# Kernel tuning notes

Hardware: AMD Instinct MI355X
Metric: run time of the kernel (lower is better)

The kernel has to match this reference:

```python
import jax, jax.numpy as jnp
import numpy as np

N_NODES = 100000
N_EDGES = 625000
HIDDEN = 128
N_LAYERS = 4
NUM_GRAPHS = 512
INPUT_DIM = 28
EDGE_DIM = 4
OUT_DIM = 1


def setup_inputs() -> dict:
    key = jax.random.key(0)
    ks = jax.random.split(key, 16)
    x = jax.random.randint(ks[0], (N_NODES, 1), 0, INPUT_DIM)
    edge_index = jax.random.randint(ks[1], (2, N_EDGES), 0, N_NODES)
    edge_attr = jax.random.randint(ks[2], (N_EDGES,), 0, EDGE_DIM)
    batch = jnp.sort(jax.random.randint(ks[3], (N_NODES,), 0, NUM_GRAPHS))
    s = 1.0 / np.sqrt(HIDDEN)
    node_emb = jax.random.normal(ks[4], (INPUT_DIM, HIDDEN), jnp.float32)
    edge_emb = jax.random.normal(ks[5], (EDGE_DIM, HIDDEN), jnp.float32)
    conv_W1 = jax.random.normal(ks[6], (N_LAYERS, HIDDEN, HIDDEN), jnp.float32) * s
    conv_b1 = jnp.zeros((N_LAYERS, HIDDEN), jnp.float32)
    conv_W2 = jax.random.normal(ks[7], (N_LAYERS, HIDDEN, HIDDEN), jnp.float32) * s
    conv_b2 = jnp.zeros((N_LAYERS, HIDDEN), jnp.float32)
    mlp_W1 = jax.random.normal(ks[8], (HIDDEN, HIDDEN // 2), jnp.float32) * s
    mlp_b1 = jnp.zeros((HIDDEN // 2,), jnp.float32)
    mlp_W2 = jax.random.normal(ks[9], (HIDDEN // 2, HIDDEN // 4), jnp.float32) * (1.0 / np.sqrt(HIDDEN // 2))
    mlp_b2 = jnp.zeros((HIDDEN // 4,), jnp.float32)
    mlp_W3 = jax.random.normal(ks[10], (HIDDEN // 4, OUT_DIM), jnp.float32) * (1.0 / np.sqrt(HIDDEN // 4))
    mlp_b3 = jnp.zeros((OUT_DIM,), jnp.float32)
    return dict(x=x, edge_index=edge_index, edge_attr=edge_attr, batch=batch,
                node_emb=node_emb, edge_emb=edge_emb,
                conv_W1=conv_W1, conv_b1=conv_b1, conv_W2=conv_W2, conv_b2=conv_b2,
                mlp_W1=mlp_W1, mlp_b1=mlp_b1, mlp_W2=mlp_W2, mlp_b2=mlp_b2,
                mlp_W3=mlp_W3, mlp_b3=mlp_b3)


def reference(x, edge_index, edge_attr, batch, node_emb, edge_emb,
              conv_W1, conv_b1, conv_W2, conv_b2,
              mlp_W1, mlp_b1, mlp_W2, mlp_b2, mlp_W3, mlp_b3):
    h = node_emb[x[:, 0]]                    # [N, H] embedding lookup (x.squeeze(-1))
    _attr = edge_emb[edge_attr]              # computed in original forward but unused by GINConv
    src, dst = edge_index[0], edge_index[1]
    for l in range(N_LAYERS):
        # GINConv (eps=0): mlp((1+eps)*x + sum_{j->i} x_j)
        agg = jax.ops.segment_sum(h[src], dst, num_segments=N_NODES)  # [N, H]
        z = agg + h
        z = jax.nn.relu(z @ conv_W1[l] + conv_b1[l])
        h = z @ conv_W2[l] + conv_b2[l]
    g = jax.ops.segment_sum(h, batch, num_segments=NUM_GRAPHS)        # global_add_pool [G, H]
    g = jax.nn.relu(g @ mlp_W1 + mlp_b1)
    g = jax.nn.relu(g @ mlp_W2 + mlp_b2)
    return g @ mlp_W3 + mlp_b3               # [G, 1]
```

## Files before the change

### kernel.cpp

```cpp
#include <hip/hip_runtime.h>

#define N_NODES 100000
#define N_EDGES 625000
#define HIDDEN 128
#define NUM_GRAPHS 512
#define CAP 40
#define PADN 100096

#define BUILD_BLKS 2443
#define EMBED_BLKS 6250
#define WT_BLKS 64

typedef unsigned int uint;
typedef unsigned short ushort;
typedef short v8s __attribute__((ext_vector_type(8)));
typedef float v16f __attribute__((ext_vector_type(16)));

__device__ __forceinline__ float b2f_lo(uint u) { return __uint_as_float(u << 16); }
__device__ __forceinline__ float b2f_hi(uint u) { return __uint_as_float(u & 0xffff0000u); }
__device__ __forceinline__ uint f2b(float f) {
  uint u = __float_as_uint(f);
  return (u + 0x7fffu + ((u >> 16) & 1u)) >> 16;
}

__global__ __launch_bounds__(256) void prep_k(const int* __restrict__ src,
                                              const int* __restrict__ dst,
                                              int* __restrict__ cursor,
                                              int* __restrict__ slots,
                                              const int* __restrict__ x,
                                              const float* __restrict__ emb,
                                              ushort* __restrict__ h,
                                              const float* __restrict__ W1,
                                              const float* __restrict__ W2,
                                              ushort* __restrict__ Wt) {
  int blk = blockIdx.x;
  int tid = threadIdx.x;
  if (blk < BUILD_BLKS) {
    int e = blk * 256 + tid;
    if (e < N_EDGES) {
      int d = dst[e];
      int p = atomicAdd(&cursor[d], 1);
      if (p < CAP) slots[(size_t)d * CAP + p] = src[e];
    }
  } else if (blk < BUILD_BLKS + EMBED_BLKS) {
    int t = (blk - BUILD_BLKS) * 256 + tid;
    int n = t >> 4;
    if (n < N_NODES) {
      int c = t & 15;
      const float4* e4 = (const float4*)(emb + (size_t)x[n] * HIDDEN + c * 8);
      float4 a = e4[0], b = e4[1];
      uint4 o;
      o.x = f2b(a.x) | (f2b(a.y) << 16);
      o.y = f2b(a.z) | (f2b(a.w) << 16);
      o.z = f2b(b.x) | (f2b(b.y) << 16);
      o.w = f2b(b.z) | (f2b(b.w) << 16);
      ((uint4*)h)[t] = o;
    }
  } else {
    int wb = blk - BUILD_BLKS - EMBED_BLKS;
    int mat = wb >> 3, chunk = wb & 7;
    const float* W = ((mat & 1) ? W2 : W1) + (size_t)(mat >> 1) * 16384;
    ushort* o = Wt + (size_t)mat * 16384;
#pragma unroll
    for (int jj = 0; jj < 8; jj++) {
      int idx = chunk * 2048 + tid + 256 * jj;
      int k = idx >> 7, n = idx & 127;
      int c = n >> 5, l31 = n & 31;
      int ks = k >> 4, khalf = (k >> 3) & 1, e = k & 7;
      o[(((c * 8 + ks) << 6) + (khalf << 5) + l31) * 8 + e] = (ushort)f2b(W[idx]);
    }
  }
}

__global__ __launch_bounds__(256) void hist_k(const int* __restrict__ cursor,
                                              int* __restrict__ bins) {
  __shared__ int lb[CAP + 1];
  int tid = threadIdx.x;
  if (tid <= CAP) lb[tid] = 0;
  __syncthreads();
  int n = blockIdx.x * 256 + tid;
  if (n < N_NODES) {
    int d = cursor[n]; if (d > CAP) d = CAP;
    atomicAdd(&lb[d], 1);
  }
  __syncthreads();
  if (tid <= CAP && lb[tid] > 0) atomicAdd(&bins[tid], lb[tid]);
}

__global__ __launch_bounds__(64) void scan_k(int* __restrict__ bins) {
  int i = threadIdx.x;
  int c = (i <= CAP) ? bins[i] : 0;
  int incl = c;
#pragma unroll
  for (int off = 1; off < 64; off <<= 1) {
    int t = __shfl_up(incl, off, 64);
    if (i >= off) incl += t;
  }
  if (i <= CAP) bins[i] = incl - c;
}

__global__ __launch_bounds__(256) void scatter_k(const int* __restrict__ cursor,
                                                 int* __restrict__ bins,
                                                 int* __restrict__ perm) {
  __shared__ int lb[CAP + 1];
  __shared__ int lbase[CAP + 1];
  int tid = threadIdx.x;
  if (tid <= CAP) lb[tid] = 0;
  __syncthreads();
  int n = blockIdx.x * 256 + tid;
  int d = 0, rank = 0;
  bool real = (n < N_NODES);
  if (real) {
    d = cursor[n]; if (d > CAP) d = CAP;
    rank = atomicAdd(&lb[d], 1);
  }
  __syncthreads();
  if (tid <= CAP) {
    int c = lb[tid];
    lbase[tid] = c > 0 ? atomicAdd(&bins[tid], c) : 0;
  }
  __syncthreads();
  if (real) perm[(N_NODES - 1) - (lbase[d] + rank)] = n;
  else if (n < PADN) perm[n] = 0;
}

union U { uint4 u; v8s s; };

__device__ __forceinline__ void loadrow2(uint4 dst[2], const uint4* __restrict__ rowp,
                                         int q) {
  dst[0] = rowp[q];
  dst[1] = rowp[q + 8];
}

__device__ __forceinline__ void accum2(const uint4 u[2], float acc[2][8]) {
#pragma unroll
  for (int ks = 0; ks < 2; ks++) {
    acc[ks][0] += b2f_lo(u[ks].x); acc[ks][1] += b2f_hi(u[ks].x);
    acc[ks][2] += b2f_lo(u[ks].y); acc[ks][3] += b2f_hi(u[ks].y);
    acc[ks][4] += b2f_lo(u[ks].z); acc[ks][5] += b2f_hi(u[ks].z);
    acc[ks][6] += b2f_lo(u[ks].w); acc[ks][7] += b2f_hi(u[ks].w);
  }
}

__global__ __launch_bounds__(256, 5) void agg_k(const ushort* __restrict__ hin,
                                                const int* __restrict__ cursor,
                                                const int* __restrict__ slots,
                                                const int* __restrict__ perm,
                                                ushort* __restrict__ t1) {
  int tid = threadIdx.x;
  int lane = tid & 63;
  int w = blockIdx.x * 4 + (tid >> 6);
  int r8 = lane & 7;
  int q = lane >> 3;
  int pidx = w * 8 + r8;
  bool valid = pidx < N_NODES;
  int prow = valid ? perm[pidx] : 0;
  int deg = valid ? cursor[prow] : 0;
  if (deg > CAP) deg = CAP;
  const int4* slv = (const int4*)(slots + (size_t)prow * CAP);
  const uint4* base = (const uint4*)hin;

  float acc[2][8];
#pragma unroll
  for (int ks = 0; ks < 2; ks++)
#pragma unroll
    for (int e = 0; e < 8; e++) acc[ks][e] = 0.f;

  uint4 P0[2], P1[2], P2[2], P3[2];
  int4 ck = slv[0];
  int4 cn = slv[1];

  loadrow2(P3, base + (size_t)prow * 16, q);
  if (deg > 0) loadrow2(P0, base + (size_t)ck.x * 16, q);
  if (deg > 1) loadrow2(P1, base + (size_t)ck.y * 16, q);
  if (deg > 2) loadrow2(P2, base + (size_t)ck.z * 16, q);
  __builtin_amdgcn_sched_barrier(0);
  accum2(P3, acc);

  int j = 0;
  while (j + 4 <= deg) {
    loadrow2(P3, base + (size_t)ck.w * 16, q);
    __builtin_amdgcn_sched_barrier(0);
    accum2(P0, acc);
    int ni = (j >> 2) + 2; if (ni > 9) ni = 9;
    int4 nx = slv[ni];
    if (j + 4 < deg) loadrow2(P0, base + (size_t)cn.x * 16, q);
    __builtin_amdgcn_sched_barrier(0);
    accum2(P1, acc);
    if (j + 5 < deg) loadrow2(P1, base + (size_t)cn.y * 16, q);
    __builtin_amdgcn_sched_barrier(0);
    accum2(P2, acc);
    if (j + 6 < deg) loadrow2(P2, base + (size_t)cn.z * 16, q);
    __builtin_amdgcn_sched_barrier(0);
    accum2(P3, acc);
    ck = cn; cn = nx;
    j += 4;
  }
  if (j < deg)     accum2(P0, acc);
  if (j + 1 < deg) accum2(P1, acc);
  if (j + 2 < deg) accum2(P2, acc);

  if (valid) {
    uint4 o0, o1;
    o0.x = f2b(acc[0][0]) | (f2b(acc[0][1]) << 16);
    o0.y = f2b(acc[0][2]) | (f2b(acc[0][3]) << 16);
    o0.z = f2b(acc[0][4]) | (f2b(acc[0][5]) << 16);
    o0.w = f2b(acc[0][6]) | (f2b(acc[0][7]) << 16);
    o1.x = f2b(acc[1][0]) | (f2b(acc[1][1]) << 16);
    o1.y = f2b(acc[1][2]) | (f2b(acc[1][3]) << 16);
    o1.z = f2b(acc[1][4]) | (f2b(acc[1][5]) << 16);
    o1.w = f2b(acc[1][6]) | (f2b(acc[1][7]) << 16);
    uint4* orow = (uint4*)(t1 + (size_t)prow * HIDDEN);
    orow[q] = o0;
    orow[q + 8] = o1;
  }
}

__global__ __launch_bounds__(64, 3) void gemm_k(ushort* __restrict__ t,
                                                const ushort* __restrict__ W1f,
                                                const ushort* __restrict__ W2f,
                                                const float* __restrict__ b1,
                                                const float* __restrict__ b2) {
  int lane = threadIdx.x;
  int l31 = lane & 31;
  int khalf = lane >> 5;
  int rb = blockIdx.x * 32;

  const uint4* rowp = (const uint4*)t + (size_t)(rb + l31) * 16;
  U afr[8];
#pragma unroll
  for (int ks = 0; ks < 8; ks++) afr[ks].u = rowp[khalf + 2 * ks];

  const uint4* W1v = (const uint4*)W1f;
  v16f acc1[4] = {};
#pragma unroll
  for (int c = 0; c < 4; c++)
#pragma unroll
    for (int ks = 0; ks < 8; ks++) {
      U b; b.u = W1v[((c * 8 + ks) << 6) + lane];
      acc1[c] = __builtin_amdgcn_mfma_f32_32x32x16_bf16(b.s, afr[ks].s, acc1[c], 0, 0, 0);
    }

  uint u[4][4][2];
#pragma unroll
  for (int c = 0; c < 4; c++)
#pragma unroll
    for (int b = 0; b < 4; b++)
#pragma unroll
      for (int ap = 0; ap < 2; ap++) {
        int r0 = 2 * ap + 4 * b, r1 = r0 + 1;
        float v0 = fmaxf(acc1[c][r0] + b1[c * 32 + 2 * ap + 8 * b + 4 * khalf], 0.f);
        float v1 = fmaxf(acc1[c][r1] + b1[c * 32 + 2 * ap + 1 + 8 * b + 4 * khalf], 0.f);
        u[c][b][ap] = f2b(v0) | (f2b(v1) << 16);
      }

  uint got[4][2][2];
#pragma unroll
  for (int c = 0; c < 4; c++)
#pragma unroll
    for (int bh = 0; bh < 2; bh++)
#pragma unroll
      for (int ap = 0; ap < 2; ap++) {
        uint send = khalf ? u[c][2 * bh][ap] : u[c][2 * bh + 1][ap];
        got[c][bh][ap] = __shfl_xor(send, 32, 64);
      }

  U az[8];
#pragma unroll
  for (int ks = 0; ks < 8; ks++) {
    uint o0 = khalf ? u[ks >> 1][2 * (ks & 1) + 1][0] : u[ks >> 1][2 * (ks & 1)][0];
    uint o1 = khalf ? u[ks >> 1][2 * (ks & 1) + 1][1] : u[ks >> 1][2 * (ks & 1)][1];
    uint g0 = got[ks >> 1][ks & 1][0];
    uint g1 = got[ks >> 1][ks & 1][1];
    az[ks].u.x = khalf ? g0 : o0;
    az[ks].u.y = khalf ? g1 : o1;
    az[ks].u.z = khalf ? o0 : g0;
    az[ks].u.w = khalf ? o1 : g1;
  }

  const uint4* W2v = (const uint4*)W2f;
  v16f acc2[4] = {};
#pragma unroll
  for (int c = 0; c < 4; c++)
#pragma unroll
    for (int ks = 0; ks < 8; ks++) {
      U b; b.u = W2v[((c * 8 + ks) << 6) + lane];
      acc2[c] = __builtin_amdgcn_mfma_f32_32x32x16_bf16(az[ks].s, b.s, acc2[c], 0, 0, 0);
    }

  float bv2[4];
#pragma unroll
  for (int c = 0; c < 4; c++) bv2[c] = b2[c * 32 + l31];
#pragma unroll
  for (int c = 0; c < 4; c++) {
    int col = c * 32 + l31;
#pragma unroll
    for (int r = 0; r < 16; r++) {
      int m = (r & 3) + 8 * (r >> 2) + 4 * khalf;
      t[(size_t)(rb + m) * HIDDEN + col] = (ushort)f2b(acc2[c][r] + bv2[c]);
    }
  }
}

__global__ __launch_bounds__(256) void poolmlp_k(const ushort* __restrict__ h,
                                                 const int* __restrict__ batch,
                                                 const float* __restrict__ W1, const float* __restrict__ b1,
                                                 const float* __restrict__ W2, const float* __restrict__ b2,
                                                 const float* __restrict__ W3, const float* __restrict__ b3,
                                                 float* __restrict__ out) {
  __shared__ int se[2];
  __shared__ float red[16][16][8];
  __shared__ float gl[128];
  __shared__ float r2[64];
  __shared__ float r3[32];
  int gi = blockIdx.x, tid = threadIdx.x;
  if (tid < 2) {
    int target = gi + tid;
    int lo = 0, hi = N_NODES;
    while (lo < hi) {
      int mid = (lo + hi) >> 1;
      if (batch[mid] < target) lo = mid + 1; else hi = mid;
    }
    se[tid] = lo;
  }
  __syncthreads();
  int start = se[0], end = se[1];
  int cg = tid & 15, rg = tid >> 4;
  float acc[8] = {0.f, 0.f, 0.f, 0.f, 0.f, 0.f, 0.f, 0.f};
  for (int r = start + rg; r < end; r += 16) {
    uint4 v = ((const uint4*)h)[r * 16 + cg];
    acc[0] += b2f_lo(v.x); acc[1] += b2f_hi(v.x);
    acc[2] += b2f_lo(v.y); acc[3] += b2f_hi(v.y);
    acc[4] += b2f_lo(v.z); acc[5] += b2f_hi(v.z);
    acc[6] += b2f_lo(v.w); acc[7] += b2f_hi(v.w);
  }
#pragma unroll
  for (int j = 0; j < 8; j++) red[rg][cg][j] = acc[j];
  __syncthreads();
  if (rg == 0) {
    float s[8];
#pragma unroll
    for (int j = 0; j < 8; j++) s[j] = red[0][cg][j];
#pragma unroll
    for (int i = 1; i < 16; i++)
#pragma unroll
      for (int j = 0; j < 8; j++) s[j] += red[i][cg][j];
#pragma unroll
    for (int j = 0; j < 8; j++) gl[cg * 8 + j] = s[j];
  }
  __syncthreads();
  if (tid < 64) {
    float s = b1[tid];
    for (int k = 0; k < 128; k++) s = fmaf(gl[k], W1[k * 64 + tid], s);
    r2[tid] = fmaxf(s, 0.f);
  }
  __syncthreads();
  if (tid < 32) {
    float s2 = b2[tid];
    for (int k = 0; k < 64; k++) s2 = fmaf(r2[k], W2[k * 32 + tid], s2);
    r3[tid] = fmaxf(s2, 0.f);
  }
  __syncthreads();
  if (tid < 64) {
    float pv = (tid < 32) ? r3[tid] * W3[tid] : 0.f;
#pragma unroll
    for (int off = 32; off > 0; off >>= 1) pv += __shfl_down(pv, off);
    if (tid == 0) out[gi] = pv + b3[0];
  }
}

extern "C" void kernel_launch(void* const* d_in, const int* in_sizes, int n_in,
                              void* d_out, int out_size, void* d_ws, size_t ws_size,
                              hipStream_t stream) {
  const int* x = (const int*)d_in[0];
  const int* src = (const int*)d_in[1];
  const int* dst = src + N_EDGES;
  const int* batch = (const int*)d_in[3];
  const float* node_emb = (const float*)d_in[4];
  const float* cW1 = (const float*)d_in[6];
  const float* cb1 = (const float*)d_in[7];
  const float* cW2 = (const float*)d_in[8];
  const float* cb2 = (const float*)d_in[9];
  const float* mW1 = (const float*)d_in[10];
  const float* mb1 = (const float*)d_in[11];
  const float* mW2 = (const float*)d_in[12];
  const float* mb2 = (const float*)d_in[13];
  const float* mW3 = (const float*)d_in[14];
  const float* mb3 = (const float*)d_in[15];
  float* out = (float*)d_out;

  char* p = (char*)d_ws;
  const size_t HB = (size_t)N_NODES * HIDDEN * sizeof(ushort);
  ushort* h = (ushort*)p;      p += HB;
  ushort* t0 = (ushort*)p;     p += HB;
  ushort* Wtb = (ushort*)p;    p += (size_t)8 * 16384 * sizeof(ushort);
  int* cursor = (int*)p;       p += (size_t)N_NODES * sizeof(int);
  int* bins = (int*)p;         p += 64 * sizeof(int);
  int* slots = (int*)p;        p += (size_t)N_NODES * CAP * sizeof(int);
  int* perm = (int*)p;         p += (size_t)PADN * sizeof(int);

  (void)hipMemsetAsync(cursor, 0, ((size_t)N_NODES + 64) * sizeof(int), stream);
  prep_k<<<BUILD_BLKS + EMBED_BLKS + WT_BLKS, 256, 0, stream>>>(
      src, dst, cursor, slots, x, node_emb, h, cW1, cW2, Wtb);
  hist_k<<<PADN / 256, 256, 0, stream>>>(cursor, bins);
  scan_k<<<1, 64, 0, stream>>>(bins);
  scatter_k<<<PADN / 256, 256, 0, stream>>>(cursor, bins, perm);

  ushort* bufs[2] = {h, t0};
  for (int l = 0; l < 4; l++) {
    ushort* in = bufs[l & 1];
    ushort* tmp = bufs[(l & 1) ^ 1];
    agg_k<<<PADN / 32, 256, 0, stream>>>(in, cursor, slots, perm, tmp);
    gemm_k<<<N_NODES / 32, 64, 0, stream>>>(tmp,
                                            Wtb + (size_t)(2 * l) * 16384,
                                            Wtb + (size_t)(2 * l + 1) * 16384,
                                            cb1 + (size_t)l * HIDDEN,
                                            cb2 + (size_t)l * HIDDEN);
  }
  poolmlp_k<<<NUM_GRAPHS, 256, 0, stream>>>(h, batch, mW1, mb1, mW2, mb2, mW3, mb3, out);
}
```

Measured before the change: 358.9 us.

## Split hidden features into column slices for cache-local gather in aggregation

Node features move from row-major layout to eight 16-feature slices, each stored contiguously across nodes. Each aggregation block now handles one slice for 256 nodes, one node per thread. Because blockIdx.x & 7 picks the slice, consecutive blocks work on different slices over the same node group, which is meant to keep the gathered rows of one slice (3.2 MB) resident in cache and cut scattered-gather traffic. Embedding, GEMM load/store and pooling index arithmetic are updated to match, and nontemporal hints are added. In exchange, perm, cursor and slot lists are re-read once per slice, and the GEMM's scattered 2-byte output stores may get costlier.

```diff
diff --git a/kernel.cpp b/kernel.cpp
--- a/kernel.cpp
+++ b/kernel.cpp
@@ -15,6 +15,11 @@
 typedef unsigned short ushort;
 typedef short v8s __attribute__((ext_vector_type(8)));
 typedef float v16f __attribute__((ext_vector_type(16)));
+typedef int v4i __attribute__((ext_vector_type(4)));
+typedef uint v4u __attribute__((ext_vector_type(4)));
+
+#define SL_U4 ((size_t)N_NODES * 2)
+#define SL_US ((size_t)N_NODES * 16)
 
 __device__ __forceinline__ float b2f_lo(uint u) { return __uint_as_float(u << 16); }
 __device__ __forceinline__ float b2f_hi(uint u) { return __uint_as_float(u & 0xffff0000u); }
@@ -54,7 +59,7 @@
       o.y = f2b(a.z) | (f2b(a.w) << 16);
       o.z = f2b(b.x) | (f2b(b.y) << 16);
       o.w = f2b(b.z) | (f2b(b.w) << 16);
-      ((uint4*)h)[t] = o;
+      ((uint4*)h)[(size_t)(c >> 1) * SL_U4 + (size_t)n * 2 + (c & 1)] = o;
     }
   } else {
     int wb = blk - BUILD_BLKS - EMBED_BLKS;
@@ -126,94 +131,85 @@
 
 union U { uint4 u; v8s s; };
 
-__device__ __forceinline__ void loadrow2(uint4 dst[2], const uint4* __restrict__ rowp,
-                                         int q) {
-  dst[0] = rowp[q];
-  dst[1] = rowp[q + 8];
-}
-
-__device__ __forceinline__ void accum2(const uint4 u[2], float acc[2][8]) {
-#pragma unroll
-  for (int ks = 0; ks < 2; ks++) {
-    acc[ks][0] += b2f_lo(u[ks].x); acc[ks][1] += b2f_hi(u[ks].x);
-    acc[ks][2] += b2f_lo(u[ks].y); acc[ks][3] += b2f_hi(u[ks].y);
-    acc[ks][4] += b2f_lo(u[ks].z); acc[ks][5] += b2f_hi(u[ks].z);
-    acc[ks][6] += b2f_lo(u[ks].w); acc[ks][7] += b2f_hi(u[ks].w);
-  }
-}
-
-__global__ __launch_bounds__(256, 5) void agg_k(const ushort* __restrict__ hin,
+__device__ __forceinline__ void ld2(uint4 d[2], const uint4* __restrict__ rp) {
+  d[0] = rp[0];
+  d[1] = rp[1];
+}
+
+__device__ __forceinline__ void ac2(const uint4 u[2], float acc[16]) {
+#pragma unroll
+  for (int k = 0; k < 2; k++) {
+    acc[k * 8 + 0] += b2f_lo(u[k].x); acc[k * 8 + 1] += b2f_hi(u[k].x);
+    acc[k * 8 + 2] += b2f_lo(u[k].y); acc[k * 8 + 3] += b2f_hi(u[k].y);
+    acc[k * 8 + 4] += b2f_lo(u[k].z); acc[k * 8 + 5] += b2f_hi(u[k].z);
+    acc[k * 8 + 6] += b2f_lo(u[k].w); acc[k * 8 + 7] += b2f_hi(u[k].w);
+  }
+}
+
+__global__ __launch_bounds__(256, 4) void agg_k(const ushort* __restrict__ hin,
                                                 const int* __restrict__ cursor,
                                                 const int* __restrict__ slots,
                                                 const int* __restrict__ perm,
                                                 ushort* __restrict__ t1) {
-  int tid = threadIdx.x;
-  int lane = tid & 63;
-  int w = blockIdx.x * 4 + (tid >> 6);
-  int r8 = lane & 7;
-  int q = lane >> 3;
-  int pidx = w * 8 + r8;
-  bool valid = pidx < N_NODES;
-  int prow = valid ? perm[pidx] : 0;
-  int deg = valid ? cursor[prow] : 0;
+  int s = blockIdx.x & 7;
+  int g = blockIdx.x >> 3;
+  int pidx = g * 256 + threadIdx.x;
+  if (pidx >= N_NODES) return;
+  int prow = __builtin_nontemporal_load(perm + pidx);
+  int deg = __builtin_nontemporal_load(cursor + prow);
   if (deg > CAP) deg = CAP;
-  const int4* slv = (const int4*)(slots + (size_t)prow * CAP);
-  const uint4* base = (const uint4*)hin;
-
-  float acc[2][8];
-#pragma unroll
-  for (int ks = 0; ks < 2; ks++)
-#pragma unroll
-    for (int e = 0; e < 8; e++) acc[ks][e] = 0.f;
-
+  const uint4* sb = (const uint4*)hin + (size_t)s * SL_U4;
+  const v4i* slv = (const v4i*)(slots + (size_t)prow * CAP);
+
+  float acc[16];
   uint4 P0[2], P1[2], P2[2], P3[2];
-  int4 ck = slv[0];
-  int4 cn = slv[1];
-
-  loadrow2(P3, base + (size_t)prow * 16, q);
-  if (deg > 0) loadrow2(P0, base + (size_t)ck.x * 16, q);
-  if (deg > 1) loadrow2(P1, base + (size_t)ck.y * 16, q);
-  if (deg > 2) loadrow2(P2, base + (size_t)ck.z * 16, q);
+  v4i ck = __builtin_nontemporal_load(slv);
+  v4i cn = __builtin_nontemporal_load(slv + 1);
+
+  ld2(P3, sb + (size_t)prow * 2);
+  if (deg > 0) ld2(P0, sb + (size_t)ck[0] * 2);
+  if (deg > 1) ld2(P1, sb + (size_t)ck[1] * 2);
+  if (deg > 2) ld2(P2, sb + (size_t)ck[2] * 2);
   __builtin_amdgcn_sched_barrier(0);
-  accum2(P3, acc);
+#pragma unroll
+  for (int e = 0; e < 16; e++) acc[e] = 0.f;
+  ac2(P3, acc);
 
   int j = 0;
   while (j + 4 <= deg) {
-    loadrow2(P3, base + (size_t)ck.w * 16, q);
+    ld2(P3, sb + (size_t)ck[3] * 2);
     __builtin_amdgcn_sched_barrier(0);
-    accum2(P0, acc);
+    ac2(P0, acc);
     int ni = (j >> 2) + 2; if (ni > 9) ni = 9;
-    int4 nx = slv[ni];
-    if (j + 4 < deg) loadrow2(P0, base + (size_t)cn.x * 16, q);
+    v4i nx = __builtin_nontemporal_load(slv + ni);
+    if (j + 4 < deg) ld2(P0, sb + (size_t)cn[0] * 2);
     __builtin_amdgcn_sched_barrier(0);
-    accum2(P1, acc);
-    if (j + 5 < deg) loadrow2(P1, base + (size_t)cn.y * 16, q);
+    ac2(P1, acc);
+    if (j + 5 < deg) ld2(P1, sb + (size_t)cn[1] * 2);
     __builtin_amdgcn_sched_barrier(0);
-    accum2(P2, acc);
-    if (j + 6 < deg) loadrow2(P2, base + (size_t)cn.z * 16, q);
+    ac2(P2, acc);
+    if (j + 6 < deg) ld2(P2, sb + (size_t)cn[2] * 2);
     __builtin_amdgcn_sched_barrier(0);
-    accum2(P3, acc);
+    ac2(P3, acc);
     ck = cn; cn = nx;
     j += 4;
   }
-  if (j < deg)     accum2(P0, acc);
-  if (j + 1 < deg) accum2(P1, acc);
-  if (j + 2 < deg) accum2(P2, acc);
-
-  if (valid) {
-    uint4 o0, o1;
-    o0.x = f2b(acc[0][0]) | (f2b(acc[0][1]) << 16);
-    o0.y = f2b(acc[0][2]) | (f2b(acc[0][3]) << 16);
-    o0.z = f2b(acc[0][4]) | (f2b(acc[0][5]) << 16);
-    o0.w = f2b(acc[0][6]) | (f2b(acc[0][7]) << 16);
-    o1.x = f2b(acc[1][0]) | (f2b(acc[1][1]) << 16);
-    o1.y = f2b(acc[1][2]) | (f2b(acc[1][3]) << 16);
-    o1.z = f2b(acc[1][4]) | (f2b(acc[1][5]) << 16);
-    o1.w = f2b(acc[1][6]) | (f2b(acc[1][7]) << 16);
-    uint4* orow = (uint4*)(t1 + (size_t)prow * HIDDEN);
-    orow[q] = o0;
-    orow[q + 8] = o1;
-  }
+  if (j < deg)     ac2(P0, acc);
+  if (j + 1 < deg) ac2(P1, acc);
+  if (j + 2 < deg) ac2(P2, acc);
+
+  v4u o0, o1;
+  o0[0] = f2b(acc[0])  | (f2b(acc[1])  << 16);
+  o0[1] = f2b(acc[2])  | (f2b(acc[3])  << 16);
+  o0[2] = f2b(acc[4])  | (f2b(acc[5])  << 16);
+  o0[3] = f2b(acc[6])  | (f2b(acc[7])  << 16);
+  o1[0] = f2b(acc[8])  | (f2b(acc[9])  << 16);
+  o1[1] = f2b(acc[10]) | (f2b(acc[11]) << 16);
+  o1[2] = f2b(acc[12]) | (f2b(acc[13]) << 16);
+  o1[3] = f2b(acc[14]) | (f2b(acc[15]) << 16);
+  v4u* orow = (v4u*)(t1 + (size_t)s * SL_US + (size_t)prow * 16);
+  __builtin_nontemporal_store(o0, orow);
+  __builtin_nontemporal_store(o1, orow + 1);
 }
 
 __global__ __launch_bounds__(64, 3) void gemm_k(ushort* __restrict__ t,
@@ -226,10 +222,11 @@
   int khalf = lane >> 5;
   int rb = blockIdx.x * 32;
 
-  const uint4* rowp = (const uint4*)t + (size_t)(rb + l31) * 16;
+  const uint4* tv = (const uint4*)t;
   U afr[8];
 #pragma unroll
-  for (int ks = 0; ks < 8; ks++) afr[ks].u = rowp[khalf + 2 * ks];
+  for (int ks = 0; ks < 8; ks++)
+    afr[ks].u = tv[(size_t)ks * SL_U4 + (size_t)(rb + l31) * 2 + khalf];
 
   const uint4* W1v = (const uint4*)W1f;
   v16f acc1[4] = {};
@@ -293,11 +290,12 @@
   for (int c = 0; c < 4; c++) bv2[c] = b2[c * 32 + l31];
 #pragma unroll
   for (int c = 0; c < 4; c++) {
-    int col = c * 32 + l31;
+    int sc = (c << 1) + (l31 >> 4);
+    int cw = l31 & 15;
 #pragma unroll
     for (int r = 0; r < 16; r++) {
       int m = (r & 3) + 8 * (r >> 2) + 4 * khalf;
-      t[(size_t)(rb + m) * HIDDEN + col] = (ushort)f2b(acc2[c][r] + bv2[c]);
+      t[(size_t)sc * SL_US + (size_t)(rb + m) * 16 + cw] = (ushort)f2b(acc2[c][r] + bv2[c]);
     }
   }
 }
@@ -327,8 +325,9 @@
   int start = se[0], end = se[1];
   int cg = tid & 15, rg = tid >> 4;
   float acc[8] = {0.f, 0.f, 0.f, 0.f, 0.f, 0.f, 0.f, 0.f};
+  size_t sbase = (size_t)(cg >> 1) * SL_U4 + (cg & 1);
   for (int r = start + rg; r < end; r += 16) {
-    uint4 v = ((const uint4*)h)[r * 16 + cg];
+    uint4 v = ((const uint4*)h)[sbase + (size_t)r * 2];
     acc[0] += b2f_lo(v.x); acc[1] += b2f_hi(v.x);
     acc[2] += b2f_lo(v.y); acc[3] += b2f_hi(v.y);
     acc[4] += b2f_lo(v.z); acc[5] += b2f_hi(v.z);
@@ -410,7 +409,7 @@
   for (int l = 0; l < 4; l++) {
     ushort* in = bufs[l & 1];
     ushort* tmp = bufs[(l & 1) ^ 1];
-    agg_k<<<PADN / 32, 256, 0, stream>>>(in, cursor, slots, perm, tmp);
+    agg_k<<<8 * (PADN / 256), 256, 0, stream>>>(in, cursor, slots, perm, tmp);
     gemm_k<<<N_NODES / 32, 64, 0, stream>>>(tmp,
                                             Wtb + (size_t)(2 * l) * 16384,
                                             Wtb + (size_t)(2 * l + 1) * 16384,
```

After: 641.2 us. +78.7%, slower.
